# Performance work log

Measured on AMD Instinct MI355X. Metric: run time of the kernel, lower is better.

The kernel has to match this reference:

```python
import jax, jax.numpy as jnp
import numpy as np

N = 100_000      # nodes
E = 3_200_000    # edges (avg degree 32)
D_IN = 128
D_H = 128
EPS = 1e-12      # F.normalize eps


def setup_inputs() -> dict:
    key = jax.random.key(0)
    k1, k2, k3 = jax.random.split(key, 3)
    X = jax.random.normal(k1, (N, D_IN), dtype=jnp.float32)
    edge_index = jax.random.randint(k2, (2, E), 0, N, dtype=jnp.int32)
    # GCNConv linear weight (stored as [in, out] for X @ W) and bias
    W = jax.random.normal(k3, (D_IN, D_H), dtype=jnp.float32) / np.sqrt(D_IN)
    b = jnp.zeros((D_H,), dtype=jnp.float32)
    # MessageNorm learnable scale, init 1.0
    scale = jnp.ones((1,), dtype=jnp.float32)
    return {"X": X, "edge_index": edge_index, "W": W, "b": b, "scale": scale}


def reference(X, edge_index, W, b, scale):
    n = X.shape[0]
    loop = jnp.arange(n, dtype=edge_index.dtype)
    src = jnp.concatenate([edge_index[0], loop])  # add self loops
    tgt = jnp.concatenate([edge_index[1], loop])
    # symmetric GCN normalization: D^{-1/2} (A+I) D^{-1/2}
    deg = jax.ops.segment_sum(jnp.ones_like(src, X.dtype), tgt, num_segments=n)
    dinv = jnp.where(deg > 0, jax.lax.rsqrt(deg), 0.0)
    norm = dinv[src] * dinv[tgt]  # [E+N]
    XW = X @ W  # [N, D_H]
    msg = jax.ops.segment_sum(norm[:, None] * XW[src], tgt, num_segments=n) + b
    # MessageNorm(learn_scale=True): l2-normalize msg, rescale by ||x||_2 * scale
    msg_n = msg / jnp.maximum(jnp.linalg.norm(msg, axis=-1, keepdims=True), EPS)
    x_norm = jnp.linalg.norm(X, axis=-1, keepdims=True)
    return jax.nn.gelu(msg_n * x_norm * scale, approximate=False)
```

## Files before the change

### kernel.cpp

```cpp
#include <hip/hip_runtime.h>
#include <math.h>

#define D 128
#define NB 391
#define BSH 8
#define BMASK 255
#define CAP 10240
#define EPB 4096
#define LDA 136

typedef unsigned short ushort_t;
typedef unsigned int uint_t;
typedef __attribute__((ext_vector_type(8))) short bfrag;
typedef __attribute__((ext_vector_type(4))) float ffrag;

__device__ inline ushort_t f2bf(float f) {
    uint_t u = __float_as_uint(f);
    uint_t r = (u + 0x7FFFu + ((u >> 16) & 1u)) >> 16;
    return (ushort_t)r;
}

__global__ __launch_bounds__(256) void k_wt(const float* __restrict__ W,
                                            ushort_t* __restrict__ Wt) {
    __shared__ float T[32][33];
    int bi = blockIdx.x >> 2, bj = blockIdx.x & 3;
    int tid = threadIdx.x;
    int r = tid >> 3;
    int c4 = tid & 7;
    float4 v = *(const float4*)&W[(size_t)(bi * 32 + r) * D + bj * 32 + c4 * 4];
    T[r][c4 * 4 + 0] = v.x; T[r][c4 * 4 + 1] = v.y;
    T[r][c4 * 4 + 2] = v.z; T[r][c4 * 4 + 3] = v.w;
    __syncthreads();
    int cc = (tid & 7) * 4;
    ushort4 o;
    o.x = f2bf(T[cc + 0][r]); o.y = f2bf(T[cc + 1][r]);
    o.z = f2bf(T[cc + 2][r]); o.w = f2bf(T[cc + 3][r]);
    *(ushort4*)&Wt[(size_t)(bj * 32 + r) * D + bi * 32 + cc] = o;
}

__global__ __launch_bounds__(256) void k_bin(const int* __restrict__ src,
                                             const int* __restrict__ tgt, int e,
                                             int* __restrict__ bucket_cur,
                                             uint_t* __restrict__ binned) {
    __shared__ int lcnt[NB];
    __shared__ int lbase[NB];
    int tid = threadIdx.x;
    int base = blockIdx.x * EPB;
    for (int i = tid; i < NB; i += 256) lcnt[i] = 0;
    __syncthreads();

    int myb[16], myrank[16];
    uint_t myval[16];
#pragma unroll
    for (int k = 0; k < 16; ++k) {
        int i = base + k * 256 + tid;
        if (i < e) {
            int t = tgt[i];
            int s = src[i];
            int b = t >> BSH;
            myb[k] = b;
            myval[k] = ((uint_t)s << BSH) | (uint_t)(t & BMASK);
            myrank[k] = atomicAdd(&lcnt[b], 1);
        } else {
            myb[k] = -1;
        }
    }
    __syncthreads();
    for (int i = tid; i < NB; i += 256) {
        int c = lcnt[i];
        lbase[i] = (c > 0) ? atomicAdd(&bucket_cur[i], c) : 0;
    }
    __syncthreads();
#pragma unroll
    for (int k = 0; k < 16; ++k) {
        if (myb[k] >= 0) {
            int slot = lbase[myb[k]] + myrank[k];
            if (slot < CAP) binned[(size_t)myb[k] * CAP + slot] = myval[k];
        }
    }
}

__global__ void k_bscan(const int* __restrict__ bucket_cur, int* __restrict__ bucket_base) {
    __shared__ int sm[512];
    int tid = threadIdx.x;
    int v = (tid < NB) ? min(bucket_cur[tid], CAP) : 0;
    sm[tid] = v;
    __syncthreads();
    int x = v;
    for (int off = 1; off < 512; off <<= 1) {
        int y = (tid >= off) ? sm[tid - off] : 0;
        __syncthreads();
        x += y;
        sm[tid] = x;
        __syncthreads();
    }
    if (tid < NB) bucket_base[tid] = x - v;
}

__global__ __launch_bounds__(256) void k_sort(const uint_t* __restrict__ binned,
                                              const int* __restrict__ bucket_cur,
                                              const int* __restrict__ bucket_base,
                                              int* __restrict__ col,
                                              int* __restrict__ rowptr,
                                              float* __restrict__ dinv, int n) {
    __shared__ uint_t sout[CAP];
    __shared__ int scnt[256];
    __shared__ int sincl[256];
    __shared__ int sofs[256];
    int b = blockIdx.x;
    int tid = threadIdx.x;
    int nb = min(bucket_cur[b], CAP);
    int baseg = bucket_base[b];
    const uint_t* bin = binned + (size_t)b * CAP;

    scnt[tid] = 0;
    __syncthreads();
    for (int i = tid; i < nb; i += 256)
        atomicAdd(&scnt[bin[i] & BMASK], 1);
    __syncthreads();
    int x = scnt[tid];
    sincl[tid] = x;
    __syncthreads();
    for (int off = 1; off < 256; off <<= 1) {
        int y = (tid >= off) ? sincl[tid - off] : 0;
        __syncthreads();
        x += y;
        sincl[tid] = x;
        __syncthreads();
    }
    sofs[tid] = x - scnt[tid];
    int t = (b << BSH) + tid;
    if (t < n) {
        rowptr[t + 1] = baseg + x;
        dinv[t] = rsqrtf((float)scnt[tid] + 1.0f);
    }
    if (b == 0 && tid == 0) rowptr[0] = 0;
    __syncthreads();
    for (int i = tid; i < nb; i += 256) {
        uint_t v = bin[i];
        int r = atomicAdd(&sofs[v & BMASK], 1);
        sout[r] = v >> BSH;
    }
    __syncthreads();
    for (int i = tid; i < nb; i += 256)
        col[baseg + i] = (int)sout[i];
}

__global__ __launch_bounds__(256) void k_gemm(const float* __restrict__ X,
                                              const ushort_t* __restrict__ Wt,
                                              const float* __restrict__ dinv,
                                              ushort_t* __restrict__ Y,
                                              float* __restrict__ xnorm, int n) {
    __shared__ ushort_t As[64 * LDA];
    __shared__ ushort_t Bs[128 * LDA];
    int tid = threadIdx.x;
    int row0 = blockIdx.x * 64;

    for (int i = tid; i < 128 * 16; i += 256) {
        int nr = i >> 4, c = (i & 15) << 3;
        *(uint4*)&Bs[nr * LDA + c] = *(const uint4*)&Wt[(size_t)nr * D + c];
    }

    const float4* X4 = (const float4*)X;
#pragma unroll
    for (int i2 = 0; i2 < 8; ++i2) {
        int item = i2 * 256 + tid;
        int r = item >> 5, c4 = item & 31;
        int gr = row0 + r;
        float4 v = (gr < n) ? X4[(size_t)gr * 32 + c4] : make_float4(0.f, 0.f, 0.f, 0.f);
        ushort4 bv;
        bv.x = f2bf(v.x); bv.y = f2bf(v.y); bv.z = f2bf(v.z); bv.w = f2bf(v.w);
        *(ushort4*)&As[r * LDA + c4 * 4] = bv;
        float s = v.x * v.x + v.y * v.y + v.z * v.z + v.w * v.w;
        s += __shfl_xor(s, 1);
        s += __shfl_xor(s, 2);
        s += __shfl_xor(s, 4);
        s += __shfl_xor(s, 8);
        s += __shfl_xor(s, 16);
        if ((tid & 31) == 0 && gr < n) xnorm[gr] = sqrtf(s);
    }
    __syncthreads();

    int w = tid >> 6;
    int lane = tid & 63;
    int q = lane >> 4;
    int mi = lane & 15;

    bfrag af[4];
#pragma unroll
    for (int kt = 0; kt < 4; ++kt)
        af[kt] = *(const bfrag*)&As[(w * 16 + mi) * LDA + kt * 32 + q * 8];

    ffrag acc[8];
#pragma unroll
    for (int nt = 0; nt < 8; ++nt) acc[nt] = (ffrag){0.f, 0.f, 0.f, 0.f};

#pragma unroll
    for (int nt = 0; nt < 8; ++nt) {
#pragma unroll
        for (int kt = 0; kt < 4; ++kt) {
            bfrag bf_ = *(const bfrag*)&Bs[(nt * 16 + mi) * LDA + kt * 32 + q * 8];
            acc[nt] = __builtin_amdgcn_mfma_f32_16x16x32_bf16(af[kt], bf_, acc[nt], 0, 0, 0);
        }
    }

    float dv[4];
#pragma unroll
    for (int i = 0; i < 4; ++i) {
        int gr = row0 + w * 16 + q * 4 + i;
        dv[i] = (gr < n) ? dinv[gr] : 0.f;
    }
#pragma unroll
    for (int nt = 0; nt < 8; ++nt) {
        int cn = nt * 16 + mi;
#pragma unroll
        for (int i = 0; i < 4; ++i) {
            int gr = row0 + w * 16 + q * 4 + i;
            if (gr < n) Y[(size_t)gr * D + cn] = f2bf(acc[nt][i] * dv[i]);
        }
    }
}

__global__ __launch_bounds__(256) void k_agg(const ushort_t* __restrict__ Y,
                                             const float* __restrict__ xnorm,
                                             const float* __restrict__ dinv,
                                             const int* __restrict__ rowptr,
                                             const int* __restrict__ col,
                                             const float* __restrict__ bias,
                                             const float* __restrict__ scale,
                                             float* __restrict__ out, int n) {
    int t = (blockIdx.x * 256 + threadIdx.x) >> 6;
    int lane = threadIdx.x & 63;
    if (t >= n) return;

    const char* Yb = (const char*)Y;
    uint_t lo4 = (uint_t)lane * 4;

    uint_t p = *(const uint_t*)(Yb + (((uint_t)t << 8) + lo4));
    float a0 = __uint_as_float(p << 16);
    float a1 = __uint_as_float(p & 0xFFFF0000u);

    int beg = rowptr[t];
    int end = rowptr[t + 1];
    int e = beg;
    for (; e + 8 <= end; e += 8) {
        int s0 = col[e],     s1 = col[e + 1], s2 = col[e + 2], s3 = col[e + 3];
        int s4 = col[e + 4], s5 = col[e + 5], s6 = col[e + 6], s7 = col[e + 7];
        uint_t q0 = *(const uint_t*)(Yb + (((uint_t)s0 << 8) + lo4));
        uint_t q1 = *(const uint_t*)(Yb + (((uint_t)s1 << 8) + lo4));
        uint_t q2 = *(const uint_t*)(Yb + (((uint_t)s2 << 8) + lo4));
        uint_t q3 = *(const uint_t*)(Yb + (((uint_t)s3 << 8) + lo4));
        uint_t q4 = *(const uint_t*)(Yb + (((uint_t)s4 << 8) + lo4));
        uint_t q5 = *(const uint_t*)(Yb + (((uint_t)s5 << 8) + lo4));
        uint_t q6 = *(const uint_t*)(Yb + (((uint_t)s6 << 8) + lo4));
        uint_t q7 = *(const uint_t*)(Yb + (((uint_t)s7 << 8) + lo4));
        a0 += __uint_as_float(q0 << 16);  a1 += __uint_as_float(q0 & 0xFFFF0000u);
        a0 += __uint_as_float(q1 << 16);  a1 += __uint_as_float(q1 & 0xFFFF0000u);
        a0 += __uint_as_float(q2 << 16);  a1 += __uint_as_float(q2 & 0xFFFF0000u);
        a0 += __uint_as_float(q3 << 16);  a1 += __uint_as_float(q3 & 0xFFFF0000u);
        a0 += __uint_as_float(q4 << 16);  a1 += __uint_as_float(q4 & 0xFFFF0000u);
        a0 += __uint_as_float(q5 << 16);  a1 += __uint_as_float(q5 & 0xFFFF0000u);
        a0 += __uint_as_float(q6 << 16);  a1 += __uint_as_float(q6 & 0xFFFF0000u);
        a0 += __uint_as_float(q7 << 16);  a1 += __uint_as_float(q7 & 0xFFFF0000u);
    }
    for (; e < end; ++e) {
        int s = col[e];
        uint_t q = *(const uint_t*)(Yb + (((uint_t)s << 8) + lo4));
        a0 += __uint_as_float(q << 16);
        a1 += __uint_as_float(q & 0xFFFF0000u);
    }

    float dt = dinv[t];
    float m0 = fmaf(dt, a0, bias[lane * 2]);
    float m1 = fmaf(dt, a1, bias[lane * 2 + 1]);

    float m2 = m0 * m0 + m1 * m1;
#pragma unroll
    for (int m = 32; m >= 1; m >>= 1) m2 += __shfl_xor(m2, m);

    float denom = fmaxf(sqrtf(m2), 1e-12f);
    float fac = xnorm[t] * scale[0] / denom;
    float g0 = m0 * fac;
    float g1 = m1 * fac;
    float2 o;
    o.x = 0.5f * g0 * (1.0f + erff(g0 * 0.70710678118654752440f));
    o.y = 0.5f * g1 * (1.0f + erff(g1 * 0.70710678118654752440f));
    *(float2*)&out[(size_t)t * D + lane * 2] = o;
}


extern "C" void kernel_launch(void* const* d_in, const int* in_sizes, int n_in,
                              void* d_out, int out_size, void* d_ws, size_t ws_size,
                              hipStream_t stream) {
    const float* X     = (const float*)d_in[0];
    const int*   ei    = (const int*)d_in[1];
    const float* W     = (const float*)d_in[2];
    const float* bias  = (const float*)d_in[3];
    const float* scale = (const float*)d_in[4];
    float* out = (float*)d_out;

    int n = in_sizes[0] / D;
    int e = in_sizes[1] / 2;
    const int* src = ei;
    const int* tgt = ei + e;

    char* ws = (char*)d_ws;
    ushort_t* Y = (ushort_t*)ws;   ws += (size_t)n * D * sizeof(ushort_t);
    uint_t* binned = (uint_t*)Y;
    float* dinv = (float*)ws;      ws += (size_t)n * sizeof(float);
    float* xnorm = (float*)ws;     ws += (size_t)n * sizeof(float);
    int* rowptr = (int*)ws;        ws += (size_t)(n + 1) * sizeof(int);
    int* bucket_cur = (int*)ws;    ws += NB * sizeof(int);
    int* bucket_base = (int*)ws;   ws += NB * sizeof(int);
    int* col = (int*)ws;           ws += (size_t)e * sizeof(int);
    ushort_t* Wt = (ushort_t*)ws;

    hipMemsetAsync(bucket_cur, 0, NB * sizeof(int), stream);
    k_wt<<<16, 256, 0, stream>>>(W, Wt);
    k_bin<<<(e + EPB - 1) / EPB, 256, 0, stream>>>(src, tgt, e, bucket_cur, binned);
    k_bscan<<<1, 512, 0, stream>>>(bucket_cur, bucket_base);
    k_sort<<<NB, 256, 0, stream>>>(binned, bucket_cur, bucket_base, col, rowptr, dinv, n);
    k_gemm<<<(n + 63) / 64, 256, 0, stream>>>(X, Wt, dinv, Y, xnorm, n);
    k_agg<<<(n + 3) / 4, 256, 0, stream>>>(Y, xnorm, dinv, rowptr, col, bias, scale, out, n);
}
```

Before: 329.0 us.

## Fuse weight transpose and bucket scan into neighbors, vectorize GEMM stores, deepen gather unroll

Folds the W transpose into the first blocks of the binning kernel and replaces the separate bucket prefix-scan kernel with a per-block reduction inside the sort kernel, removing two launches. The GEMM swaps its MFMA operands so each lane holds four consecutive columns of one row, which allows packed ushort4 stores of Y instead of scattered 2-byte stores. The aggregation gather loop is unrolled to 16 neighbours with a 4-wide remainder loop to keep more loads in flight. In exchange, every sort block now redundantly sums up to 391 bucket counts, and the transpose inside the bin kernel reads W with strided, uncoalesced loads.

```diff
diff --git a/kernel.cpp b/kernel.cpp
--- a/kernel.cpp
+++ b/kernel.cpp
@@ -20,31 +20,27 @@
     return (ushort_t)r;
 }
 
-__global__ __launch_bounds__(256) void k_wt(const float* __restrict__ W,
-                                            ushort_t* __restrict__ Wt) {
-    __shared__ float T[32][33];
-    int bi = blockIdx.x >> 2, bj = blockIdx.x & 3;
-    int tid = threadIdx.x;
-    int r = tid >> 3;
-    int c4 = tid & 7;
-    float4 v = *(const float4*)&W[(size_t)(bi * 32 + r) * D + bj * 32 + c4 * 4];
-    T[r][c4 * 4 + 0] = v.x; T[r][c4 * 4 + 1] = v.y;
-    T[r][c4 * 4 + 2] = v.z; T[r][c4 * 4 + 3] = v.w;
-    __syncthreads();
-    int cc = (tid & 7) * 4;
-    ushort4 o;
-    o.x = f2bf(T[cc + 0][r]); o.y = f2bf(T[cc + 1][r]);
-    o.z = f2bf(T[cc + 2][r]); o.w = f2bf(T[cc + 3][r]);
-    *(ushort4*)&Wt[(size_t)(bj * 32 + r) * D + bi * 32 + cc] = o;
-}
-
 __global__ __launch_bounds__(256) void k_bin(const int* __restrict__ src,
                                              const int* __restrict__ tgt, int e,
                                              int* __restrict__ bucket_cur,
-                                             uint_t* __restrict__ binned) {
+                                             uint_t* __restrict__ binned,
+                                             const float* __restrict__ W,
+                                             ushort_t* __restrict__ Wt) {
     __shared__ int lcnt[NB];
     __shared__ int lbase[NB];
     int tid = threadIdx.x;
+
+    if (blockIdx.x < 16) {
+        int nrow = blockIdx.x * 8 + (tid >> 5);
+        int k0 = (tid & 31) * 4;
+        ushort4 o;
+        o.x = f2bf(W[(size_t)(k0 + 0) * D + nrow]);
+        o.y = f2bf(W[(size_t)(k0 + 1) * D + nrow]);
+        o.z = f2bf(W[(size_t)(k0 + 2) * D + nrow]);
+        o.w = f2bf(W[(size_t)(k0 + 3) * D + nrow]);
+        *(ushort4*)&Wt[(size_t)nrow * D + k0] = o;
+    }
+
     int base = blockIdx.x * EPB;
     for (int i = tid; i < NB; i += 256) lcnt[i] = 0;
     __syncthreads();
@@ -80,26 +76,8 @@
     }
 }
 
-__global__ void k_bscan(const int* __restrict__ bucket_cur, int* __restrict__ bucket_base) {
-    __shared__ int sm[512];
-    int tid = threadIdx.x;
-    int v = (tid < NB) ? min(bucket_cur[tid], CAP) : 0;
-    sm[tid] = v;
-    __syncthreads();
-    int x = v;
-    for (int off = 1; off < 512; off <<= 1) {
-        int y = (tid >= off) ? sm[tid - off] : 0;
-        __syncthreads();
-        x += y;
-        sm[tid] = x;
-        __syncthreads();
-    }
-    if (tid < NB) bucket_base[tid] = x - v;
-}
-
 __global__ __launch_bounds__(256) void k_sort(const uint_t* __restrict__ binned,
                                               const int* __restrict__ bucket_cur,
-                                              const int* __restrict__ bucket_base,
                                               int* __restrict__ col,
                                               int* __restrict__ rowptr,
                                               float* __restrict__ dinv, int n) {
@@ -107,10 +85,21 @@
     __shared__ int scnt[256];
     __shared__ int sincl[256];
     __shared__ int sofs[256];
+    __shared__ int sred[256];
     int b = blockIdx.x;
     int tid = threadIdx.x;
+
+    int v = 0;
+    for (int i = tid; i < b; i += 256) v += min(bucket_cur[i], CAP);
+    sred[tid] = v;
+    __syncthreads();
+    for (int off = 128; off >= 1; off >>= 1) {
+        if (tid < off) sred[tid] += sred[tid + off];
+        __syncthreads();
+    }
+    int baseg = sred[0];
+
     int nb = min(bucket_cur[b], CAP);
-    int baseg = bucket_base[b];
     const uint_t* bin = binned + (size_t)b * CAP;
 
     scnt[tid] = 0;
@@ -137,9 +126,9 @@
     if (b == 0 && tid == 0) rowptr[0] = 0;
     __syncthreads();
     for (int i = tid; i < nb; i += 256) {
-        uint_t v = bin[i];
-        int r = atomicAdd(&sofs[v & BMASK], 1);
-        sout[r] = v >> BSH;
+        uint_t w = bin[i];
+        int r = atomicAdd(&sofs[w & BMASK], 1);
+        sout[r] = w >> BSH;
     }
     __syncthreads();
     for (int i = tid; i < nb; i += 256)
@@ -186,10 +175,10 @@
     int q = lane >> 4;
     int mi = lane & 15;
 
-    bfrag af[4];
+    bfrag xf[4];
 #pragma unroll
     for (int kt = 0; kt < 4; ++kt)
-        af[kt] = *(const bfrag*)&As[(w * 16 + mi) * LDA + kt * 32 + q * 8];
+        xf[kt] = *(const bfrag*)&As[(w * 16 + mi) * LDA + kt * 32 + q * 8];
 
     ffrag acc[8];
 #pragma unroll
@@ -199,24 +188,22 @@
     for (int nt = 0; nt < 8; ++nt) {
 #pragma unroll
         for (int kt = 0; kt < 4; ++kt) {
-            bfrag bf_ = *(const bfrag*)&Bs[(nt * 16 + mi) * LDA + kt * 32 + q * 8];
-            acc[nt] = __builtin_amdgcn_mfma_f32_16x16x32_bf16(af[kt], bf_, acc[nt], 0, 0, 0);
-        }
-    }
-
-    float dv[4];
-#pragma unroll
-    for (int i = 0; i < 4; ++i) {
-        int gr = row0 + w * 16 + q * 4 + i;
-        dv[i] = (gr < n) ? dinv[gr] : 0.f;
-    }
-#pragma unroll
-    for (int nt = 0; nt < 8; ++nt) {
-        int cn = nt * 16 + mi;
-#pragma unroll
-        for (int i = 0; i < 4; ++i) {
-            int gr = row0 + w * 16 + q * 4 + i;
-            if (gr < n) Y[(size_t)gr * D + cn] = f2bf(acc[nt][i] * dv[i]);
+            bfrag wf = *(const bfrag*)&Bs[(nt * 16 + mi) * LDA + kt * 32 + q * 8];
+            acc[nt] = __builtin_amdgcn_mfma_f32_16x16x32_bf16(wf, xf[kt], acc[nt], 0, 0, 0);
+        }
+    }
+
+    int gr = row0 + w * 16 + mi;
+    if (gr < n) {
+        float dv = dinv[gr];
+#pragma unroll
+        for (int nt = 0; nt < 8; ++nt) {
+            ushort4 o;
+            o.x = f2bf(acc[nt][0] * dv);
+            o.y = f2bf(acc[nt][1] * dv);
+            o.z = f2bf(acc[nt][2] * dv);
+            o.w = f2bf(acc[nt][3] * dv);
+            *(ushort4*)&Y[(size_t)gr * D + nt * 16 + q * 4] = o;
         }
     }
 }
@@ -243,25 +230,31 @@
     int beg = rowptr[t];
     int end = rowptr[t + 1];
     int e = beg;
-    for (; e + 8 <= end; e += 8) {
-        int s0 = col[e],     s1 = col[e + 1], s2 = col[e + 2], s3 = col[e + 3];
-        int s4 = col[e + 4], s5 = col[e + 5], s6 = col[e + 6], s7 = col[e + 7];
-        uint_t q0 = *(const uint_t*)(Yb + (((uint_t)s0 << 8) + lo4));
-        uint_t q1 = *(const uint_t*)(Yb + (((uint_t)s1 << 8) + lo4));
-        uint_t q2 = *(const uint_t*)(Yb + (((uint_t)s2 << 8) + lo4));
-        uint_t q3 = *(const uint_t*)(Yb + (((uint_t)s3 << 8) + lo4));
-        uint_t q4 = *(const uint_t*)(Yb + (((uint_t)s4 << 8) + lo4));
-        uint_t q5 = *(const uint_t*)(Yb + (((uint_t)s5 << 8) + lo4));
-        uint_t q6 = *(const uint_t*)(Yb + (((uint_t)s6 << 8) + lo4));
-        uint_t q7 = *(const uint_t*)(Yb + (((uint_t)s7 << 8) + lo4));
-        a0 += __uint_as_float(q0 << 16);  a1 += __uint_as_float(q0 & 0xFFFF0000u);
-        a0 += __uint_as_float(q1 << 16);  a1 += __uint_as_float(q1 & 0xFFFF0000u);
-        a0 += __uint_as_float(q2 << 16);  a1 += __uint_as_float(q2 & 0xFFFF0000u);
-        a0 += __uint_as_float(q3 << 16);  a1 += __uint_as_float(q3 & 0xFFFF0000u);
-        a0 += __uint_as_float(q4 << 16);  a1 += __uint_as_float(q4 & 0xFFFF0000u);
-        a0 += __uint_as_float(q5 << 16);  a1 += __uint_as_float(q5 & 0xFFFF0000u);
-        a0 += __uint_as_float(q6 << 16);  a1 += __uint_as_float(q6 & 0xFFFF0000u);
-        a0 += __uint_as_float(q7 << 16);  a1 += __uint_as_float(q7 & 0xFFFF0000u);
+    for (; e + 16 <= end; e += 16) {
+        uint_t qv[16];
+#pragma unroll
+        for (int k = 0; k < 16; ++k) {
+            int s = col[e + k];
+            qv[k] = *(const uint_t*)(Yb + (((uint_t)s << 8) + lo4));
+        }
+#pragma unroll
+        for (int k = 0; k < 16; ++k) {
+            a0 += __uint_as_float(qv[k] << 16);
+            a1 += __uint_as_float(qv[k] & 0xFFFF0000u);
+        }
+    }
+    for (; e + 4 <= end; e += 4) {
+        uint_t qv[4];
+#pragma unroll
+        for (int k = 0; k < 4; ++k) {
+            int s = col[e + k];
+            qv[k] = *(const uint_t*)(Yb + (((uint_t)s << 8) + lo4));
+        }
+#pragma unroll
+        for (int k = 0; k < 4; ++k) {
+            a0 += __uint_as_float(qv[k] << 16);
+            a1 += __uint_as_float(qv[k] & 0xFFFF0000u);
+        }
     }
     for (; e < end; ++e) {
         int s = col[e];
@@ -311,15 +304,12 @@
     float* xnorm = (float*)ws;     ws += (size_t)n * sizeof(float);
     int* rowptr = (int*)ws;        ws += (size_t)(n + 1) * sizeof(int);
     int* bucket_cur = (int*)ws;    ws += NB * sizeof(int);
-    int* bucket_base = (int*)ws;   ws += NB * sizeof(int);
     int* col = (int*)ws;           ws += (size_t)e * sizeof(int);
     ushort_t* Wt = (ushort_t*)ws;
 
     hipMemsetAsync(bucket_cur, 0, NB * sizeof(int), stream);
-    k_wt<<<16, 256, 0, stream>>>(W, Wt);
-    k_bin<<<(e + EPB - 1) / EPB, 256, 0, stream>>>(src, tgt, e, bucket_cur, binned);
-    k_bscan<<<1, 512, 0, stream>>>(bucket_cur, bucket_base);
-    k_sort<<<NB, 256, 0, stream>>>(binned, bucket_cur, bucket_base, col, rowptr, dinv, n);
+    k_bin<<<(e + EPB - 1) / EPB, 256, 0, stream>>>(src, tgt, e, bucket_cur, binned, W, Wt);
+    k_sort<<<NB, 256, 0, stream>>>(binned, bucket_cur, col, rowptr, dinv, n);
     k_gemm<<<(n + 63) / 64, 256, 0, stream>>>(X, Wt, dinv, Y, xnorm, n);
     k_agg<<<(n + 3) / 4, 256, 0, stream>>>(Y, xnorm, dinv, rowptr, col, bias, scale, out, n);
 }
```

Measured after the change: 309.5 us. 1.06x faster.
